# Kernel optimization log

Hardware: AMD Instinct MI355X
Metric: run time of the kernel (lower is better)

## Reference

```python
import jax, jax.numpy as jnp
import numpy as np

N_NODES = 50000
N_EDGES = 800000
D_IN, D_HID, D_OUT = 128, 64, 64


def gcn_conv(x, W, b, src, dst, num_nodes):
    """PyG-style GCNConv: add self-loops, symmetric norm, aggregate at target.
    src/dst already include self-loops. x: [N, Din], W: [Din, Dout]."""
    xw = x @ W  # transform first (Din -> Dout), like PyG
    ew = jnp.ones(src.shape[0], dtype=x.dtype)
    deg = jax.ops.segment_sum(ew, dst, num_segments=num_nodes)
    dis = jnp.where(deg > 0, jax.lax.rsqrt(deg), 0.0)  # deg^{-1/2}
    norm = dis[src] * ew * dis[dst]  # [E+N]
    msgs = norm[:, None] * xw[src]  # gather source features
    out = jax.ops.segment_sum(msgs, dst, num_segments=num_nodes)
    return out + b


def setup_inputs() -> dict:
    key = jax.random.key(0)
    ks = jax.random.split(key, 8)
    x = jax.random.normal(ks[0], (N_NODES, D_IN), dtype=jnp.float32)
    edge_index = jax.random.randint(ks[1], (2, N_EDGES), 0, N_NODES, dtype=jnp.int64)
    W1 = jax.random.normal(ks[2], (D_IN, D_HID), dtype=jnp.float32) * (1.0 / np.sqrt(D_IN))
    b1 = jnp.zeros((D_HID,), dtype=jnp.float32)
    W2 = jax.random.normal(ks[3], (D_HID, D_HID), dtype=jnp.float32) * (1.0 / np.sqrt(D_HID))
    b2 = jnp.zeros((D_HID,), dtype=jnp.float32)
    W3 = jax.random.normal(ks[4], (D_HID, D_OUT), dtype=jnp.float32) * (1.0 / np.sqrt(D_HID))
    b3 = jnp.zeros((D_OUT,), dtype=jnp.float32)
    return {"x": x, "edge_index": edge_index, "W1": W1, "b1": b1,
            "W2": W2, "b2": b2, "W3": W3, "b3": b3}


def reference(x, edge_index, W1, b1, W2, b2, W3, b3):
    # Add self-loops once (shared by all layers), as PyG GCNConv does per layer.
    loop = jnp.arange(N_NODES, dtype=edge_index.dtype)
    src = jnp.concatenate([edge_index[0], loop])
    dst = jnp.concatenate([edge_index[1], loop])
    # Layer 1 + ReLU (dropout is identity in eval mode)
    h = gcn_conv(x, W1, b1, src, dst, N_NODES)
    h = jax.nn.relu(h)
    # Layer 2 + ReLU
    h = gcn_conv(h, W2, b2, src, dst, N_NODES)
    h = jax.nn.relu(h)
    # Layer 3 (no activation)
    out = gcn_conv(h, W3, b3, src, dst, N_NODES)
    return out
```

## Files before the change

### kernel.cpp

```cpp
#include <hip/hip_runtime.h>
#include <hip/hip_fp16.h>

#define N_NODES 50000
#define N_PAD   50048
#define N_EDGES 800000
#define E_TOT   (N_EDGES + N_NODES)
#define D_IN    128
#define D_HID   64

#define NB       196
#define EB_CHUNK 4096

typedef __bf16 bf16x8 __attribute__((ext_vector_type(8)));
typedef __bf16 bf16x4 __attribute__((ext_vector_type(4)));
typedef float  f32x4  __attribute__((ext_vector_type(4)));


__global__ __launch_bounds__(256) void k_binc(const int* __restrict__ dst,
                                              unsigned* __restrict__ bucket_cnt) {
  __shared__ unsigned lh[256];
  int t = threadIdx.x;
  lh[t] = 0;
  __syncthreads();
  int base = blockIdx.x * EB_CHUNK;
  int endv = min(base + EB_CHUNK, N_EDGES);
  for (int e = base + t; e < endv; e += 256)
    atomicAdd(&lh[((unsigned)dst[e]) >> 8], 1u);
  __syncthreads();
  if (t < NB && lh[t]) atomicAdd(&bucket_cnt[t], lh[t]);
}

__global__ __launch_bounds__(256) void k_bscan(const unsigned* __restrict__ bucket_cnt,
                                               unsigned* __restrict__ bucket_ebase,
                                               unsigned* __restrict__ bucket_fill,
                                               unsigned* __restrict__ bucket_cbase,
                                               unsigned* __restrict__ rowptr) {
  __shared__ unsigned se[256], sc[256];
  int t = threadIdx.x;
  unsigned cnt   = (t < NB) ? bucket_cnt[t] : 0u;
  unsigned nodes = (t < NB) ? (unsigned)min(256, N_NODES - t * 256) : 0u;
  unsigned ctot  = cnt + nodes;
  se[t] = cnt; sc[t] = ctot;
  __syncthreads();
  for (int off = 1; off < 256; off <<= 1) {
    unsigned a = (t >= off) ? se[t - off] : 0u;
    unsigned b = (t >= off) ? sc[t - off] : 0u;
    __syncthreads();
    se[t] += a; sc[t] += b;
    __syncthreads();
  }
  if (t < NB) {
    bucket_ebase[t] = se[t] - cnt;
    bucket_fill[t]  = se[t] - cnt;
    bucket_cbase[t] = sc[t] - ctot;
  }
  if (t == 0) rowptr[N_NODES] = E_TOT;
}

__global__ __launch_bounds__(256) void k_bins(const int* __restrict__ src,
                                              const int* __restrict__ dst,
                                              unsigned* __restrict__ bucket_fill,
                                              unsigned* __restrict__ temp) {
  __shared__ unsigned lh[256], lcur[256];
  int t = threadIdx.x;
  lh[t] = 0;
  __syncthreads();
  int base = blockIdx.x * EB_CHUNK;
  int endv = min(base + EB_CHUNK, N_EDGES);
  for (int e = base + t; e < endv; e += 256)
    atomicAdd(&lh[((unsigned)dst[e]) >> 8], 1u);
  __syncthreads();
  if (t < NB && lh[t]) lcur[t] = atomicAdd(&bucket_fill[t], lh[t]);
  __syncthreads();
  for (int e = base + t; e < endv; e += 256) {
    unsigned d = (unsigned)dst[e];
    unsigned b = d >> 8;
    unsigned pos = atomicAdd(&lcur[b], 1u);
    temp[pos] = (unsigned)src[e] | ((d & 255u) << 16);
  }
}

__global__ __launch_bounds__(256) void k_csr(const unsigned* __restrict__ temp,
                                             const unsigned* __restrict__ bucket_ebase,
                                             const unsigned* __restrict__ bucket_cnt,
                                             const unsigned* __restrict__ bucket_cbase,
                                             unsigned* __restrict__ rowptr,
                                             float* __restrict__ dis,
                                             unsigned* __restrict__ csr) {
  __shared__ unsigned hist[256], sscan[256], lfill[256];
  int b = blockIdx.x, t = threadIdx.x;
  unsigned ebase = bucket_ebase[b], ecnt = bucket_cnt[b], cbase = bucket_cbase[b];
  int nodes = min(256, N_NODES - b * 256);
  hist[t] = 0;
  __syncthreads();
  for (unsigned i = t; i < ecnt; i += 256)
    atomicAdd(&hist[(temp[ebase + i] >> 16) & 255u], 1u);
  __syncthreads();
  unsigned deg = (t < nodes) ? hist[t] + 1u : 0u;
  sscan[t] = deg;
  __syncthreads();
  for (int off = 1; off < 256; off <<= 1) {
    unsigned x = (t >= off) ? sscan[t - off] : 0u;
    __syncthreads();
    sscan[t] += x;
    __syncthreads();
  }
  unsigned excl = sscan[t] - deg;
  if (t < nodes) {
    int node = b * 256 + t;
    rowptr[node] = cbase + excl;
    dis[node] = rsqrtf((float)deg);
    csr[cbase + excl] = (unsigned)node;
  }
  lfill[t] = excl + 1u;
  __syncthreads();
  for (unsigned i = t; i < ecnt; i += 256) {
    unsigned v = temp[ebase + i];
    unsigned d = (v >> 16) & 255u;
    unsigned pos = atomicAdd(&lfill[d], 1u);
    csr[cbase + pos] = v & 0xFFFFu;
  }
}


template <int K>
__device__ inline void pack_w(const float* __restrict__ W,
                              __bf16* __restrict__ Bh, __bf16* __restrict__ Bl, int i) {
  constexpr int KS = K / 32;
  int j = i & 7, lane = (i >> 3) & 63, rest = i >> 9;
  int ct = rest / KS, ks = rest - ct * KS;
  int k = ks * 32 + ((lane >> 4) << 3) + j;
  int c = ct * 16 + (lane & 15);
  float v = W[k * 64 + c];
  __bf16 hb = (__bf16)v;
  Bh[i] = hb;
  Bl[i] = (__bf16)(v - (float)hb);
}

__global__ __launch_bounds__(256) void k_split_w3(const float* __restrict__ W1,
                                                  const float* __restrict__ W2,
                                                  const float* __restrict__ W3,
                                                  __bf16* __restrict__ Wh1, __bf16* __restrict__ Wl1,
                                                  __bf16* __restrict__ Wh2, __bf16* __restrict__ Wl2,
                                                  __bf16* __restrict__ Wh3, __bf16* __restrict__ Wl3) {
  int b = blockIdx.x, t = threadIdx.x;
  if (b < 32)      pack_w<D_IN >(W1, Wh1, Wl1, b * 256 + t);
  else if (b < 48) pack_w<D_HID>(W2, Wh2, Wl2, (b - 32) * 256 + t);
  else             pack_w<D_HID>(W3, Wh3, Wl3, (b - 48) * 256 + t);
}


template <int K, bool FIRST>
__global__ __launch_bounds__(256) void k_gemm_mfma(const float* __restrict__ Xf,
                                                   const __bf16* __restrict__ Ah,
                                                   const __bf16* __restrict__ Al,
                                                   const __bf16* __restrict__ Bh,
                                                   const __bf16* __restrict__ Bl,
                                                   __half* __restrict__ Y) {
  constexpr int KS = K / 32;
  const int tid  = threadIdx.x;
  const int wave = tid >> 6;
  const int lane = tid & 63;
  const int row0 = blockIdx.x * 64 + wave * 16;
  const int row_a = FIRST ? min(row0 + (lane & 15), N_NODES - 1)
                          : row0 + (lane & 15);
  const int q8 = (lane >> 4) << 3;

  f32x4 acc[4];
#pragma unroll
  for (int ct = 0; ct < 4; ct++) acc[ct] = (f32x4){0.f, 0.f, 0.f, 0.f};

#pragma unroll
  for (int ks = 0; ks < KS; ks++) {
    bf16x8 ah, al;
    if (FIRST) {
      const float4* xr4 = reinterpret_cast<const float4*>(Xf + (size_t)row_a * K);
      float4 f0 = xr4[ks * 8 + (q8 >> 2) + 0];
      float4 f1 = xr4[ks * 8 + (q8 >> 2) + 1];
#pragma unroll
      for (int j = 0; j < 4; j++) {
        float a0 = (&f0.x)[j], a1 = (&f1.x)[j];
        __bf16 h0 = (__bf16)a0, h1 = (__bf16)a1;
        ah[j] = h0;     al[j] = (__bf16)(a0 - (float)h0);
        ah[4 + j] = h1; al[4 + j] = (__bf16)(a1 - (float)h1);
      }
    } else {
      size_t abase = (size_t)row_a * K + q8 + ks * 32;
      ah = *reinterpret_cast<const bf16x8*>(Ah + abase);
      al = *reinterpret_cast<const bf16x8*>(Al + abase);
    }
#pragma unroll
    for (int ct = 0; ct < 4; ct++) {
      bf16x8 bh = *reinterpret_cast<const bf16x8*>(Bh + (size_t)((ct * KS + ks) * 64 + lane) * 8);
      bf16x8 bl = *reinterpret_cast<const bf16x8*>(Bl + (size_t)((ct * KS + ks) * 64 + lane) * 8);
      acc[ct] = __builtin_amdgcn_mfma_f32_16x16x32_bf16(ah, bh, acc[ct], 0, 0, 0);
      acc[ct] = __builtin_amdgcn_mfma_f32_16x16x32_bf16(ah, bl, acc[ct], 0, 0, 0);
      acc[ct] = __builtin_amdgcn_mfma_f32_16x16x32_bf16(al, bh, acc[ct], 0, 0, 0);
    }
  }

  const int rbase = row0 + ((lane >> 4) << 2);
  const int c     = lane & 15;
#pragma unroll
  for (int ct = 0; ct < 4; ct++)
#pragma unroll
    for (int r = 0; r < 4; r++) {
      int row = rbase + r;
      if (row < N_NODES)
        Y[(size_t)row * 64 + ct * 16 + c] = __float2half_rn(acc[ct][r]);
    }
}


template <int MODE>
__global__ __launch_bounds__(256) void k_agg(const uint2* __restrict__ XW2,
                                             const unsigned* __restrict__ rowptr,
                                             const unsigned* __restrict__ csr,
                                             const float* __restrict__ dis,
                                             const float4* __restrict__ bias4,
                                             __bf16* __restrict__ hh,
                                             __bf16* __restrict__ hl,
                                             float4* __restrict__ OUT4) {
  int node = (int)((blockIdx.x * blockDim.x + threadIdx.x) >> 6);
  int lane = threadIdx.x & 63;
  if (node >= N_NODES) return;
  const int sub = lane & 15;
  const int grp = lane >> 4;

  const float disd = dis[node];
  unsigned beg = rowptr[node], end = rowptr[node + 1];
  float4 acc0 = {0.f, 0.f, 0.f, 0.f};
  float4 acc1 = {0.f, 0.f, 0.f, 0.f};

  for (unsigned j = beg; j < end; j += 64) {
    int nj = (int)min(64u, end - j);
    unsigned s = 0u; float nrm = 0.f;
    if (lane < nj) {
      s = csr[j + lane];
      nrm = dis[s] * disd;
    }
    for (int k = 0; k < nj; k += 8) {
      int e0 = k + grp, e1 = k + grp + 4;
      unsigned s0 = (unsigned)__shfl((int)s, e0);
      float    n0 = __shfl(nrm, e0);
      unsigned s1 = (unsigned)__shfl((int)s, e1);
      float    n1 = __shfl(nrm, e1);
      uint2 v0 = XW2[(size_t)s0 * 16 + sub];
      uint2 v1 = XW2[(size_t)s1 * 16 + sub];
      float2 a01 = __half22float2(*reinterpret_cast<__half2*>(&v0.x));
      float2 a23 = __half22float2(*reinterpret_cast<__half2*>(&v0.y));
      float2 b01 = __half22float2(*reinterpret_cast<__half2*>(&v1.x));
      float2 b23 = __half22float2(*reinterpret_cast<__half2*>(&v1.y));
      acc0.x += n0 * a01.x; acc0.y += n0 * a01.y; acc0.z += n0 * a23.x; acc0.w += n0 * a23.y;
      acc1.x += n1 * b01.x; acc1.y += n1 * b01.y; acc1.z += n1 * b23.x; acc1.w += n1 * b23.y;
    }
  }

  float4 acc;
  acc.x = acc0.x + acc1.x; acc.y = acc0.y + acc1.y;
  acc.z = acc0.z + acc1.z; acc.w = acc0.w + acc1.w;
  acc.x += __shfl_xor(acc.x, 16); acc.y += __shfl_xor(acc.y, 16);
  acc.z += __shfl_xor(acc.z, 16); acc.w += __shfl_xor(acc.w, 16);
  acc.x += __shfl_xor(acc.x, 32); acc.y += __shfl_xor(acc.y, 32);
  acc.z += __shfl_xor(acc.z, 32); acc.w += __shfl_xor(acc.w, 32);

  if (grp == 0) {
    float4 b = bias4[sub];
    acc.x += b.x; acc.y += b.y; acc.z += b.z; acc.w += b.w;
    if (MODE == 0) {
      acc.x = fmaxf(acc.x, 0.f); acc.y = fmaxf(acc.y, 0.f);
      acc.z = fmaxf(acc.z, 0.f); acc.w = fmaxf(acc.w, 0.f);
      bf16x4 hv, lv;
#pragma unroll
      for (int cidx = 0; cidx < 4; cidx++) {
        float f = (&acc.x)[cidx];
        __bf16 hb = (__bf16)f;
        hv[cidx] = hb;
        lv[cidx] = (__bf16)(f - (float)hb);
      }
      *reinterpret_cast<bf16x4*>(&hh[(size_t)node * 64 + sub * 4]) = hv;
      *reinterpret_cast<bf16x4*>(&hl[(size_t)node * 64 + sub * 4]) = lv;
    } else {
      OUT4[(size_t)node * 16 + sub] = acc;
    }
  }
}


extern "C" void kernel_launch(void* const* d_in, const int* in_sizes, int n_in,
                              void* d_out, int out_size, void* d_ws, size_t ws_size,
                              hipStream_t stream) {
  const float* x    = (const float*)d_in[0];
  const int*   eidx = (const int*)d_in[1];
  const float* W1   = (const float*)d_in[2];
  const float* b1   = (const float*)d_in[3];
  const float* W2   = (const float*)d_in[4];
  const float* b2   = (const float*)d_in[5];
  const float* W3   = (const float*)d_in[6];
  const float* b3   = (const float*)d_in[7];
  float* out = (float*)d_out;

  const int* e_src = eidx;
  const int* e_dst = eidx + N_EDGES;

  size_t off = 0;
  auto alloc = [&](size_t bytes) -> void* {
    void* p = (char*)d_ws + off;
    off += (bytes + 255) & ~(size_t)255;
    return p;
  };
  unsigned* rowptr  = (unsigned*)alloc((size_t)(N_NODES + 1) * 4);
  float*    dis     = (float*)alloc((size_t)N_NODES * 4);
  unsigned* csr     = (unsigned*)alloc((size_t)E_TOT * 4);
  unsigned* temp    = (unsigned*)alloc((size_t)N_EDGES * 4);
  unsigned* bcnt    = (unsigned*)alloc(256 * 4);
  unsigned* bebase  = (unsigned*)alloc(256 * 4);
  unsigned* bfill   = (unsigned*)alloc(256 * 4);
  unsigned* bcbase  = (unsigned*)alloc(256 * 4);
  __half*   xw      = (__half*)alloc((size_t)N_PAD * 64 * 2);
  __bf16*   hhA     = (__bf16*)alloc((size_t)N_PAD * 64 * 2);
  __bf16*   hlA     = (__bf16*)alloc((size_t)N_PAD * 64 * 2);
  __bf16*   hhB     = (__bf16*)alloc((size_t)N_PAD * 64 * 2);
  __bf16*   hlB     = (__bf16*)alloc((size_t)N_PAD * 64 * 2);
  __bf16*   Wh1     = (__bf16*)alloc((size_t)D_IN * 64 * 2);
  __bf16*   Wl1     = (__bf16*)alloc((size_t)D_IN * 64 * 2);
  __bf16*   Wh2     = (__bf16*)alloc((size_t)D_HID * 64 * 2);
  __bf16*   Wl2     = (__bf16*)alloc((size_t)D_HID * 64 * 2);
  __bf16*   Wh3     = (__bf16*)alloc((size_t)D_HID * 64 * 2);
  __bf16*   Wl3     = (__bf16*)alloc((size_t)D_HID * 64 * 2);

  const int bin_grid = (N_EDGES + EB_CHUNK - 1) / EB_CHUNK;

  hipMemsetAsync(bcnt, 0, 256 * 4, stream);
  k_binc <<<bin_grid, 256, 0, stream>>>(e_dst, bcnt);
  k_bscan<<<1,        256, 0, stream>>>(bcnt, bebase, bfill, bcbase, rowptr);
  k_bins <<<bin_grid, 256, 0, stream>>>(e_src, e_dst, bfill, temp);
  k_csr  <<<NB,       256, 0, stream>>>(temp, bebase, bcnt, bcbase, rowptr, dis, csr);
  k_split_w3<<<64, 256, 0, stream>>>(W1, W2, W3, Wh1, Wl1, Wh2, Wl2, Wh3, Wl3);

  const int gemm_grid = N_PAD / 64;
  const int agg_grid  = (N_NODES * 64 + 255) / 256;

  k_gemm_mfma<D_IN, true><<<gemm_grid, 256, 0, stream>>>(x, nullptr, nullptr, Wh1, Wl1, xw);
  k_agg<0><<<agg_grid, 256, 0, stream>>>((const uint2*)xw, rowptr, csr, dis,
                                         (const float4*)b1, hhA, hlA, nullptr);
  k_gemm_mfma<D_HID, false><<<gemm_grid, 256, 0, stream>>>(nullptr, hhA, hlA, Wh2, Wl2, xw);
  k_agg<0><<<agg_grid, 256, 0, stream>>>((const uint2*)xw, rowptr, csr, dis,
                                         (const float4*)b2, hhB, hlB, nullptr);
  k_gemm_mfma<D_HID, false><<<gemm_grid, 256, 0, stream>>>(nullptr, hhB, hlB, Wh3, Wl3, xw);
  k_agg<1><<<agg_grid, 256, 0, stream>>>((const uint2*)xw, rowptr, csr, dis,
                                         (const float4*)b3, nullptr, nullptr, (float4*)out);
}
```

Measured before the change: 155.7 us.

## Fuse preprocessing kernels, use deterministic per-block offsets, widen aggregation loads

The weight-split kernel is merged into the binning-count kernel, and the layer-1 GEMM is merged into the CSR-build kernel. This removes a memset and two launches and lets independent work run side by side. Binning now writes per-block histograms, and a serial scan in k_bscan turns them into offsets, replacing global atomics and the duplicate histogram pass in k_bins. The aggregation kernel switches to 16-byte loads, with 8 lanes per row and 8 edges per wave step instead of 4. The cost is a serial 196-step loop in the single-block scan and more registers in the aggregation kernel.

Measured after the change: 139.7 us. 10.2% less time.

```diff
diff --git a/kernel.cpp b/kernel.cpp
--- a/kernel.cpp
+++ b/kernel.cpp
@@ -8,124 +8,17 @@
 #define D_IN    128
 #define D_HID   64
 
-#define NB       196
-#define EB_CHUNK 4096
+#define NB         196
+#define EB_CHUNK   4096
+#define BIN_BLOCKS 196
 
 typedef __bf16 bf16x8 __attribute__((ext_vector_type(8)));
-typedef __bf16 bf16x4 __attribute__((ext_vector_type(4)));
 typedef float  f32x4  __attribute__((ext_vector_type(4)));
 
 
-__global__ __launch_bounds__(256) void k_binc(const int* __restrict__ dst,
-                                              unsigned* __restrict__ bucket_cnt) {
-  __shared__ unsigned lh[256];
-  int t = threadIdx.x;
-  lh[t] = 0;
-  __syncthreads();
-  int base = blockIdx.x * EB_CHUNK;
-  int endv = min(base + EB_CHUNK, N_EDGES);
-  for (int e = base + t; e < endv; e += 256)
-    atomicAdd(&lh[((unsigned)dst[e]) >> 8], 1u);
-  __syncthreads();
-  if (t < NB && lh[t]) atomicAdd(&bucket_cnt[t], lh[t]);
-}
-
-__global__ __launch_bounds__(256) void k_bscan(const unsigned* __restrict__ bucket_cnt,
-                                               unsigned* __restrict__ bucket_ebase,
-                                               unsigned* __restrict__ bucket_fill,
-                                               unsigned* __restrict__ bucket_cbase,
-                                               unsigned* __restrict__ rowptr) {
-  __shared__ unsigned se[256], sc[256];
-  int t = threadIdx.x;
-  unsigned cnt   = (t < NB) ? bucket_cnt[t] : 0u;
-  unsigned nodes = (t < NB) ? (unsigned)min(256, N_NODES - t * 256) : 0u;
-  unsigned ctot  = cnt + nodes;
-  se[t] = cnt; sc[t] = ctot;
-  __syncthreads();
-  for (int off = 1; off < 256; off <<= 1) {
-    unsigned a = (t >= off) ? se[t - off] : 0u;
-    unsigned b = (t >= off) ? sc[t - off] : 0u;
-    __syncthreads();
-    se[t] += a; sc[t] += b;
-    __syncthreads();
-  }
-  if (t < NB) {
-    bucket_ebase[t] = se[t] - cnt;
-    bucket_fill[t]  = se[t] - cnt;
-    bucket_cbase[t] = sc[t] - ctot;
-  }
-  if (t == 0) rowptr[N_NODES] = E_TOT;
-}
-
-__global__ __launch_bounds__(256) void k_bins(const int* __restrict__ src,
-                                              const int* __restrict__ dst,
-                                              unsigned* __restrict__ bucket_fill,
-                                              unsigned* __restrict__ temp) {
-  __shared__ unsigned lh[256], lcur[256];
-  int t = threadIdx.x;
-  lh[t] = 0;
-  __syncthreads();
-  int base = blockIdx.x * EB_CHUNK;
-  int endv = min(base + EB_CHUNK, N_EDGES);
-  for (int e = base + t; e < endv; e += 256)
-    atomicAdd(&lh[((unsigned)dst[e]) >> 8], 1u);
-  __syncthreads();
-  if (t < NB && lh[t]) lcur[t] = atomicAdd(&bucket_fill[t], lh[t]);
-  __syncthreads();
-  for (int e = base + t; e < endv; e += 256) {
-    unsigned d = (unsigned)dst[e];
-    unsigned b = d >> 8;
-    unsigned pos = atomicAdd(&lcur[b], 1u);
-    temp[pos] = (unsigned)src[e] | ((d & 255u) << 16);
-  }
-}
-
-__global__ __launch_bounds__(256) void k_csr(const unsigned* __restrict__ temp,
-                                             const unsigned* __restrict__ bucket_ebase,
-                                             const unsigned* __restrict__ bucket_cnt,
-                                             const unsigned* __restrict__ bucket_cbase,
-                                             unsigned* __restrict__ rowptr,
-                                             float* __restrict__ dis,
-                                             unsigned* __restrict__ csr) {
-  __shared__ unsigned hist[256], sscan[256], lfill[256];
-  int b = blockIdx.x, t = threadIdx.x;
-  unsigned ebase = bucket_ebase[b], ecnt = bucket_cnt[b], cbase = bucket_cbase[b];
-  int nodes = min(256, N_NODES - b * 256);
-  hist[t] = 0;
-  __syncthreads();
-  for (unsigned i = t; i < ecnt; i += 256)
-    atomicAdd(&hist[(temp[ebase + i] >> 16) & 255u], 1u);
-  __syncthreads();
-  unsigned deg = (t < nodes) ? hist[t] + 1u : 0u;
-  sscan[t] = deg;
-  __syncthreads();
-  for (int off = 1; off < 256; off <<= 1) {
-    unsigned x = (t >= off) ? sscan[t - off] : 0u;
-    __syncthreads();
-    sscan[t] += x;
-    __syncthreads();
-  }
-  unsigned excl = sscan[t] - deg;
-  if (t < nodes) {
-    int node = b * 256 + t;
-    rowptr[node] = cbase + excl;
-    dis[node] = rsqrtf((float)deg);
-    csr[cbase + excl] = (unsigned)node;
-  }
-  lfill[t] = excl + 1u;
-  __syncthreads();
-  for (unsigned i = t; i < ecnt; i += 256) {
-    unsigned v = temp[ebase + i];
-    unsigned d = (v >> 16) & 255u;
-    unsigned pos = atomicAdd(&lfill[d], 1u);
-    csr[cbase + pos] = v & 0xFFFFu;
-  }
-}
-
-
 template <int K>
-__device__ inline void pack_w(const float* __restrict__ W,
-                              __bf16* __restrict__ Bh, __bf16* __restrict__ Bl, int i) {
+__device__ __forceinline__ void pack_w(const float* __restrict__ W,
+                                       __bf16* __restrict__ Bh, __bf16* __restrict__ Bl, int i) {
   constexpr int KS = K / 32;
   int j = i & 7, lane = (i >> 3) & 63, rest = i >> 9;
   int ct = rest / KS, ks = rest - ct * KS;
@@ -137,31 +30,102 @@
   Bl[i] = (__bf16)(v - (float)hb);
 }
 
-__global__ __launch_bounds__(256) void k_split_w3(const float* __restrict__ W1,
-                                                  const float* __restrict__ W2,
-                                                  const float* __restrict__ W3,
-                                                  __bf16* __restrict__ Wh1, __bf16* __restrict__ Wl1,
-                                                  __bf16* __restrict__ Wh2, __bf16* __restrict__ Wl2,
-                                                  __bf16* __restrict__ Wh3, __bf16* __restrict__ Wl3) {
-  int b = blockIdx.x, t = threadIdx.x;
-  if (b < 32)      pack_w<D_IN >(W1, Wh1, Wl1, b * 256 + t);
-  else if (b < 48) pack_w<D_HID>(W2, Wh2, Wl2, (b - 32) * 256 + t);
-  else             pack_w<D_HID>(W3, Wh3, Wl3, (b - 48) * 256 + t);
+
+__global__ __launch_bounds__(256) void k_binc_sw(const int* __restrict__ dst,
+                                                 unsigned* __restrict__ blkcnt,
+                                                 const float* __restrict__ W1,
+                                                 const float* __restrict__ W2,
+                                                 const float* __restrict__ W3,
+                                                 __bf16* __restrict__ Wh1, __bf16* __restrict__ Wl1,
+                                                 __bf16* __restrict__ Wh2, __bf16* __restrict__ Wl2,
+                                                 __bf16* __restrict__ Wh3, __bf16* __restrict__ Wl3) {
+  __shared__ unsigned lh[256];
+  int blk = blockIdx.x, t = threadIdx.x;
+  if (blk < BIN_BLOCKS) {
+    lh[t] = 0;
+    __syncthreads();
+    int base = blk * EB_CHUNK;
+    int endv = min(base + EB_CHUNK, N_EDGES);
+    for (int e = base + t; e < endv; e += 256)
+      atomicAdd(&lh[((unsigned)dst[e]) >> 8], 1u);
+    __syncthreads();
+    blkcnt[blk * 256 + t] = lh[t];
+  } else {
+    int b = blk - BIN_BLOCKS;
+    if (b < 32)      pack_w<D_IN >(W1, Wh1, Wl1, b * 256 + t);
+    else if (b < 48) pack_w<D_HID>(W2, Wh2, Wl2, (b - 32) * 256 + t);
+    else             pack_w<D_HID>(W3, Wh3, Wl3, (b - 48) * 256 + t);
+  }
+}
+
+
+__global__ __launch_bounds__(256) void k_bscan(const unsigned* __restrict__ blkcnt,
+                                               unsigned* __restrict__ blkoff,
+                                               unsigned* __restrict__ bucket_cnt,
+                                               unsigned* __restrict__ bucket_ebase,
+                                               unsigned* __restrict__ bucket_cbase,
+                                               unsigned* __restrict__ rowptr) {
+  __shared__ unsigned se[256], sc[256];
+  int t = threadIdx.x;
+  unsigned run = 0;
+  for (int b = 0; b < BIN_BLOCKS; b++) {
+    unsigned c = blkcnt[b * 256 + t];
+    blkoff[b * 256 + t] = run;
+    run += c;
+  }
+  bucket_cnt[t] = run;
+  unsigned cnt   = (t < NB) ? run : 0u;
+  unsigned nodes = (t < NB) ? (unsigned)min(256, N_NODES - t * 256) : 0u;
+  unsigned ctot  = cnt + nodes;
+  se[t] = cnt; sc[t] = ctot;
+  __syncthreads();
+  for (int off = 1; off < 256; off <<= 1) {
+    unsigned a = (t >= off) ? se[t - off] : 0u;
+    unsigned b = (t >= off) ? sc[t - off] : 0u;
+    __syncthreads();
+    se[t] += a; sc[t] += b;
+    __syncthreads();
+  }
+  if (t < NB) {
+    bucket_ebase[t] = se[t] - cnt;
+    bucket_cbase[t] = sc[t] - ctot;
+  }
+  if (t == 0) rowptr[N_NODES] = E_TOT;
+}
+
+
+__global__ __launch_bounds__(256) void k_bins(const int* __restrict__ src,
+                                              const int* __restrict__ dst,
+                                              const unsigned* __restrict__ bucket_ebase,
+                                              const unsigned* __restrict__ blkoff,
+                                              unsigned* __restrict__ temp) {
+  __shared__ unsigned lcur[256];
+  int blk = blockIdx.x, t = threadIdx.x;
+  lcur[t] = bucket_ebase[t] + blkoff[blk * 256 + t];
+  __syncthreads();
+  int base = blk * EB_CHUNK;
+  int endv = min(base + EB_CHUNK, N_EDGES);
+  for (int e = base + t; e < endv; e += 256) {
+    unsigned d = (unsigned)dst[e];
+    unsigned pos = atomicAdd(&lcur[d >> 8], 1u);
+    temp[pos] = (unsigned)src[e] | ((d & 255u) << 16);
+  }
 }
 
 
 template <int K, bool FIRST>
-__global__ __launch_bounds__(256) void k_gemm_mfma(const float* __restrict__ Xf,
-                                                   const __bf16* __restrict__ Ah,
-                                                   const __bf16* __restrict__ Al,
-                                                   const __bf16* __restrict__ Bh,
-                                                   const __bf16* __restrict__ Bl,
-                                                   __half* __restrict__ Y) {
+__device__ __forceinline__ void gemm_body(int bid,
+                                          const float* __restrict__ Xf,
+                                          const __bf16* __restrict__ Ah,
+                                          const __bf16* __restrict__ Al,
+                                          const __bf16* __restrict__ Bh,
+                                          const __bf16* __restrict__ Bl,
+                                          __half* __restrict__ Y) {
   constexpr int KS = K / 32;
   const int tid  = threadIdx.x;
   const int wave = tid >> 6;
   const int lane = tid & 63;
-  const int row0 = blockIdx.x * 64 + wave * 16;
+  const int row0 = bid * 64 + wave * 16;
   const int row_a = FIRST ? min(row0 + (lane & 15), N_NODES - 1)
                           : row0 + (lane & 15);
   const int q8 = (lane >> 4) << 3;
@@ -212,8 +176,68 @@
 }
 
 
+__global__ __launch_bounds__(256) void k_csr_gemm1(const unsigned* __restrict__ temp,
+                                                   const unsigned* __restrict__ bucket_ebase,
+                                                   const unsigned* __restrict__ bucket_cnt,
+                                                   const unsigned* __restrict__ bucket_cbase,
+                                                   unsigned* __restrict__ rowptr,
+                                                   float* __restrict__ dis,
+                                                   unsigned* __restrict__ csr,
+                                                   const float* __restrict__ x,
+                                                   const __bf16* __restrict__ Wh1,
+                                                   const __bf16* __restrict__ Wl1,
+                                                   __half* __restrict__ xw) {
+  __shared__ unsigned hist[256], sscan[256], lfill[256];
+  if (blockIdx.x >= NB) {
+    gemm_body<D_IN, true>(blockIdx.x - NB, x, nullptr, nullptr, Wh1, Wl1, xw);
+    return;
+  }
+  int b = blockIdx.x, t = threadIdx.x;
+  unsigned ebase = bucket_ebase[b], ecnt = bucket_cnt[b], cbase = bucket_cbase[b];
+  int nodes = min(256, N_NODES - b * 256);
+  hist[t] = 0;
+  __syncthreads();
+  for (unsigned i = t; i < ecnt; i += 256)
+    atomicAdd(&hist[(temp[ebase + i] >> 16) & 255u], 1u);
+  __syncthreads();
+  unsigned deg = (t < nodes) ? hist[t] + 1u : 0u;
+  sscan[t] = deg;
+  __syncthreads();
+  for (int off = 1; off < 256; off <<= 1) {
+    unsigned v = (t >= off) ? sscan[t - off] : 0u;
+    __syncthreads();
+    sscan[t] += v;
+    __syncthreads();
+  }
+  unsigned excl = sscan[t] - deg;
+  if (t < nodes) {
+    int node = b * 256 + t;
+    rowptr[node] = cbase + excl;
+    dis[node] = rsqrtf((float)deg);
+    csr[cbase + excl] = (unsigned)node;
+  }
+  lfill[t] = excl + 1u;
+  __syncthreads();
+  for (unsigned i = t; i < ecnt; i += 256) {
+    unsigned v = temp[ebase + i];
+    unsigned d = (v >> 16) & 255u;
+    unsigned pos = atomicAdd(&lfill[d], 1u);
+    csr[cbase + pos] = v & 0xFFFFu;
+  }
+}
+
+
+__global__ __launch_bounds__(256) void k_gemm23(const __bf16* __restrict__ Ah,
+                                                const __bf16* __restrict__ Al,
+                                                const __bf16* __restrict__ Bh,
+                                                const __bf16* __restrict__ Bl,
+                                                __half* __restrict__ Y) {
+  gemm_body<D_HID, false>(blockIdx.x, nullptr, Ah, Al, Bh, Bl, Y);
+}
+
+
 template <int MODE>
-__global__ __launch_bounds__(256) void k_agg(const uint2* __restrict__ XW2,
+__global__ __launch_bounds__(256) void k_agg(const float4* __restrict__ XW4,
                                              const unsigned* __restrict__ rowptr,
                                              const unsigned* __restrict__ csr,
                                              const float* __restrict__ dis,
@@ -224,13 +248,13 @@
   int node = (int)((blockIdx.x * blockDim.x + threadIdx.x) >> 6);
   int lane = threadIdx.x & 63;
   if (node >= N_NODES) return;
-  const int sub = lane & 15;
-  const int grp = lane >> 4;
+  const int sub = lane & 7;
+  const int grp = lane >> 3;
 
   const float disd = dis[node];
   unsigned beg = rowptr[node], end = rowptr[node + 1];
-  float4 acc0 = {0.f, 0.f, 0.f, 0.f};
-  float4 acc1 = {0.f, 0.f, 0.f, 0.f};
+  float acc0[8] = {0,0,0,0,0,0,0,0};
+  float acc1[8] = {0,0,0,0,0,0,0,0};
 
   for (unsigned j = beg; j < end; j += 64) {
     int nj = (int)min(64u, end - j);
@@ -239,49 +263,64 @@
       s = csr[j + lane];
       nrm = dis[s] * disd;
     }
-    for (int k = 0; k < nj; k += 8) {
-      int e0 = k + grp, e1 = k + grp + 4;
+    for (int k = 0; k < nj; k += 16) {
+      int e0 = k + grp;
       unsigned s0 = (unsigned)__shfl((int)s, e0);
       float    n0 = __shfl(nrm, e0);
-      unsigned s1 = (unsigned)__shfl((int)s, e1);
-      float    n1 = __shfl(nrm, e1);
-      uint2 v0 = XW2[(size_t)s0 * 16 + sub];
-      uint2 v1 = XW2[(size_t)s1 * 16 + sub];
-      float2 a01 = __half22float2(*reinterpret_cast<__half2*>(&v0.x));
-      float2 a23 = __half22float2(*reinterpret_cast<__half2*>(&v0.y));
-      float2 b01 = __half22float2(*reinterpret_cast<__half2*>(&v1.x));
-      float2 b23 = __half22float2(*reinterpret_cast<__half2*>(&v1.y));
-      acc0.x += n0 * a01.x; acc0.y += n0 * a01.y; acc0.z += n0 * a23.x; acc0.w += n0 * a23.y;
-      acc1.x += n1 * b01.x; acc1.y += n1 * b01.y; acc1.z += n1 * b23.x; acc1.w += n1 * b23.y;
-    }
-  }
-
-  float4 acc;
-  acc.x = acc0.x + acc1.x; acc.y = acc0.y + acc1.y;
-  acc.z = acc0.z + acc1.z; acc.w = acc0.w + acc1.w;
-  acc.x += __shfl_xor(acc.x, 16); acc.y += __shfl_xor(acc.y, 16);
-  acc.z += __shfl_xor(acc.z, 16); acc.w += __shfl_xor(acc.w, 16);
-  acc.x += __shfl_xor(acc.x, 32); acc.y += __shfl_xor(acc.y, 32);
-  acc.z += __shfl_xor(acc.z, 32); acc.w += __shfl_xor(acc.w, 32);
+      float4 v0 = XW4[(size_t)s0 * 8 + sub];
+      const __half2* h0 = reinterpret_cast<const __half2*>(&v0);
+#pragma unroll
+      for (int q = 0; q < 4; q++) {
+        float2 f = __half22float2(h0[q]);
+        acc0[2*q]   += n0 * f.x;
+        acc0[2*q+1] += n0 * f.y;
+      }
+      if (k + 8 < nj) {
+        int e1 = k + grp + 8;
+        unsigned s1 = (unsigned)__shfl((int)s, e1);
+        float    n1 = __shfl(nrm, e1);
+        float4 v1 = XW4[(size_t)s1 * 8 + sub];
+        const __half2* h1 = reinterpret_cast<const __half2*>(&v1);
+#pragma unroll
+        for (int q = 0; q < 4; q++) {
+          float2 f = __half22float2(h1[q]);
+          acc1[2*q]   += n1 * f.x;
+          acc1[2*q+1] += n1 * f.y;
+        }
+      }
+    }
+  }
+
+  float acc[8];
+#pragma unroll
+  for (int i = 0; i < 8; i++) acc[i] = acc0[i] + acc1[i];
+#pragma unroll
+  for (int i = 0; i < 8; i++) {
+    acc[i] += __shfl_xor(acc[i], 8);
+    acc[i] += __shfl_xor(acc[i], 16);
+    acc[i] += __shfl_xor(acc[i], 32);
+  }
 
   if (grp == 0) {
-    float4 b = bias4[sub];
-    acc.x += b.x; acc.y += b.y; acc.z += b.z; acc.w += b.w;
+    float4 ba = bias4[sub * 2], bb = bias4[sub * 2 + 1];
+    acc[0] += ba.x; acc[1] += ba.y; acc[2] += ba.z; acc[3] += ba.w;
+    acc[4] += bb.x; acc[5] += bb.y; acc[6] += bb.z; acc[7] += bb.w;
     if (MODE == 0) {
-      acc.x = fmaxf(acc.x, 0.f); acc.y = fmaxf(acc.y, 0.f);
-      acc.z = fmaxf(acc.z, 0.f); acc.w = fmaxf(acc.w, 0.f);
-      bf16x4 hv, lv;
-#pragma unroll
-      for (int cidx = 0; cidx < 4; cidx++) {
-        float f = (&acc.x)[cidx];
+      bf16x8 hv, lv;
+#pragma unroll
+      for (int i = 0; i < 8; i++) {
+        float f = fmaxf(acc[i], 0.f);
         __bf16 hb = (__bf16)f;
-        hv[cidx] = hb;
-        lv[cidx] = (__bf16)(f - (float)hb);
+        hv[i] = hb;
+        lv[i] = (__bf16)(f - (float)hb);
       }
-      *reinterpret_cast<bf16x4*>(&hh[(size_t)node * 64 + sub * 4]) = hv;
-      *reinterpret_cast<bf16x4*>(&hl[(size_t)node * 64 + sub * 4]) = lv;
+      *reinterpret_cast<bf16x8*>(&hh[(size_t)node * 64 + sub * 8]) = hv;
+      *reinterpret_cast<bf16x8*>(&hl[(size_t)node * 64 + sub * 8]) = lv;
     } else {
-      OUT4[(size_t)node * 16 + sub] = acc;
+      float4 o0 = {acc[0], acc[1], acc[2], acc[3]};
+      float4 o1 = {acc[4], acc[5], acc[6], acc[7]};
+      OUT4[(size_t)node * 16 + sub * 2]     = o0;
+      OUT4[(size_t)node * 16 + sub * 2 + 1] = o1;
     }
   }
 }
@@ -313,9 +352,10 @@
   float*    dis     = (float*)alloc((size_t)N_NODES * 4);
   unsigned* csr     = (unsigned*)alloc((size_t)E_TOT * 4);
   unsigned* temp    = (unsigned*)alloc((size_t)N_EDGES * 4);
+  unsigned* blkcnt  = (unsigned*)alloc((size_t)BIN_BLOCKS * 256 * 4);
+  unsigned* blkoff  = (unsigned*)alloc((size_t)BIN_BLOCKS * 256 * 4);
   unsigned* bcnt    = (unsigned*)alloc(256 * 4);
   unsigned* bebase  = (unsigned*)alloc(256 * 4);
-  unsigned* bfill   = (unsigned*)alloc(256 * 4);
   unsigned* bcbase  = (unsigned*)alloc(256 * 4);
   __half*   xw      = (__half*)alloc((size_t)N_PAD * 64 * 2);
   __bf16*   hhA     = (__bf16*)alloc((size_t)N_PAD * 64 * 2);
@@ -329,25 +369,21 @@
   __bf16*   Wh3     = (__bf16*)alloc((size_t)D_HID * 64 * 2);
   __bf16*   Wl3     = (__bf16*)alloc((size_t)D_HID * 64 * 2);
 
-  const int bin_grid = (N_EDGES + EB_CHUNK - 1) / EB_CHUNK;
-
-  hipMemsetAsync(bcnt, 0, 256 * 4, stream);
-  k_binc <<<bin_grid, 256, 0, stream>>>(e_dst, bcnt);
-  k_bscan<<<1,        256, 0, stream>>>(bcnt, bebase, bfill, bcbase, rowptr);
-  k_bins <<<bin_grid, 256, 0, stream>>>(e_src, e_dst, bfill, temp);
-  k_csr  <<<NB,       256, 0, stream>>>(temp, bebase, bcnt, bcbase, rowptr, dis, csr);
-  k_split_w3<<<64, 256, 0, stream>>>(W1, W2, W3, Wh1, Wl1, Wh2, Wl2, Wh3, Wl3);
-
   const int gemm_grid = N_PAD / 64;
   const int agg_grid  = (N_NODES * 64 + 255) / 256;
 
-  k_gemm_mfma<D_IN, true><<<gemm_grid, 256, 0, stream>>>(x, nullptr, nullptr, Wh1, Wl1, xw);
-  k_agg<0><<<agg_grid, 256, 0, stream>>>((const uint2*)xw, rowptr, csr, dis,
+  k_binc_sw<<<BIN_BLOCKS + 64, 256, 0, stream>>>(e_dst, blkcnt, W1, W2, W3,
+                                                 Wh1, Wl1, Wh2, Wl2, Wh3, Wl3);
+  k_bscan<<<1, 256, 0, stream>>>(blkcnt, blkoff, bcnt, bebase, bcbase, rowptr);
+  k_bins<<<BIN_BLOCKS, 256, 0, stream>>>(e_src, e_dst, bebase, blkoff, temp);
+  k_csr_gemm1<<<NB + gemm_grid, 256, 0, stream>>>(temp, bebase, bcnt, bcbase,
+                                                  rowptr, dis, csr, x, Wh1, Wl1, xw);
+  k_agg<0><<<agg_grid, 256, 0, stream>>>((const float4*)xw, rowptr, csr, dis,
                                          (const float4*)b1, hhA, hlA, nullptr);
-  k_gemm_mfma<D_HID, false><<<gemm_grid, 256, 0, stream>>>(nullptr, hhA, hlA, Wh2, Wl2, xw);
-  k_agg<0><<<agg_grid, 256, 0, stream>>>((const uint2*)xw, rowptr, csr, dis,
+  k_gemm23<<<gemm_grid, 256, 0, stream>>>(hhA, hlA, Wh2, Wl2, xw);
+  k_agg<0><<<agg_grid, 256, 0, stream>>>((const float4*)xw, rowptr, csr, dis,
                                          (const float4*)b2, hhB, hlB, nullptr);
-  k_gemm_mfma<D_HID, false><<<gemm_grid, 256, 0, stream>>>(nullptr, hhB, hlB, Wh3, Wl3, xw);
-  k_agg<1><<<agg_grid, 256, 0, stream>>>((const uint2*)xw, rowptr, csr, dis,
+  k_gemm23<<<gemm_grid, 256, 0, stream>>>(hhB, hlB, Wh3, Wl3, xw);
+  k_agg<1><<<agg_grid, 256, 0, stream>>>((const float4*)xw, rowptr, csr, dis,
                                          (const float4*)b3, nullptr, nullptr, (float4*)out);
 }
```
